# Kernel tuning notes

Measured on AMD Instinct MI355X. Metric: run time of the kernel, lower is better.

## Reference

```python
import jax, jax.numpy as jnp
import numpy as np
from jax import lax

B, T, F, H, L = 64, 2048, 128, 128, 2


def _lstm_layer(x, Wih, Whh, bih, bhh, h0, c0):
    """Single LSTM layer, torch gate order (i,f,g,o). x: [B,T,in] -> y: [B,T,H], hT, cT."""
    b = bih + bhh

    def step(carry, xt):
        h, c = carry
        gates = xt @ Wih.T + h @ Whh.T + b  # [B,4H]
        i, f, g, o = jnp.split(gates, 4, axis=-1)
        i = jax.nn.sigmoid(i)
        f = jax.nn.sigmoid(f)
        g = jnp.tanh(g)
        o = jax.nn.sigmoid(o)
        c = f * c + i * g
        h = o * jnp.tanh(c)
        return (h, c), h

    xs = jnp.swapaxes(x, 0, 1)  # [T,B,in]
    (hT, cT), ys = lax.scan(step, (h0, c0), xs)
    return jnp.swapaxes(ys, 0, 1), hT, cT


def setup_inputs() -> dict:
    key = jax.random.key(0)
    ks = jax.random.split(key, 20)
    s = 1.0 / np.sqrt(H)
    u = lambda k, shape: jax.random.uniform(k, shape, jnp.float32, -s, s)
    inp = {"x": jax.random.normal(ks[0], (B, T, F), jnp.float32)}
    i = 1
    for pre, in0 in (("enc", F), ("dec", H)):
        for l in range(L):
            d_in = in0 if l == 0 else H
            inp[f"{pre}_Wih{l}"] = u(ks[i], (4 * H, d_in)); i += 1
            inp[f"{pre}_Whh{l}"] = u(ks[i], (4 * H, H)); i += 1
            inp[f"{pre}_bih{l}"] = u(ks[i], (4 * H,)); i += 1
            inp[f"{pre}_bhh{l}"] = u(ks[i], (4 * H,)); i += 1
    inp["out_W"] = u(ks[i], (F, H)); i += 1
    inp["out_b"] = u(ks[i], (F,))
    return inp


def reference(x,
              enc_Wih0, enc_Whh0, enc_bih0, enc_bhh0,
              enc_Wih1, enc_Whh1, enc_bih1, enc_bhh1,
              dec_Wih0, dec_Whh0, dec_bih0, dec_bhh0,
              dec_Wih1, dec_Whh1, dec_bih1, dec_bhh1,
              out_W, out_b):
    z = jnp.zeros((x.shape[0], H), x.dtype)
    # encoder: 2 stacked layers, zero initial state
    y0, h0, c0 = _lstm_layer(x, enc_Wih0, enc_Whh0, enc_bih0, enc_bhh0, z, z)
    y1, h1, c1 = _lstm_layer(y0, enc_Wih1, enc_Whh1, enc_bih1, enc_bhh1, z, z)
    # decoder: zeros input, initial state = encoder final (h,c) per layer
    dec_in = jnp.zeros_like(x)  # valid since n_features == hidden_dim
    d0, _, _ = _lstm_layer(dec_in, dec_Wih0, dec_Whh0, dec_bih0, dec_bhh0, h0, c0)
    d1, _, _ = _lstm_layer(d0, dec_Wih1, dec_Whh1, dec_bih1, dec_bhh1, h1, c1)
    return d1 @ out_W.T + out_b
```

## Files before the change

kernel.cpp:

```cpp
#include <hip/hip_runtime.h>
#include <cstdint>
#include <cstddef>

typedef float    float4v __attribute__((ext_vector_type(4)));
typedef _Float16 f16x4   __attribute__((ext_vector_type(4)));
typedef _Float16 f16x8   __attribute__((ext_vector_type(8)));
typedef unsigned long long u64;
struct u64p { u64 a, b; };

#define DI __device__ __forceinline__

static const int Bsz = 64, Tlen = 2048, Hd = 128, G4 = 512;
static const int HSTR = 144;
static const int RING = 256;
static const int YSTR = 136;

DI float sigf_fast(float x) {
    float e = __builtin_amdgcn_exp2f(-1.442695041f * x);
    return __builtin_amdgcn_rcpf(1.f + e);
}
DI float tanhf_fast(float x) {
    float e = __builtin_amdgcn_exp2f(-2.885390082f * x);
    return 2.f * __builtin_amdgcn_rcpf(1.f + e) - 1.f;
}

DI void lds_barrier() {
    asm volatile("s_waitcnt lgkmcnt(0)\n\ts_barrier" ::: "memory");
}

DI void pin(f16x8& v) {
    float4v t = __builtin_bit_cast(float4v, v);
    asm volatile("" : "+v"(t));
    v = __builtin_bit_cast(f16x8, t);
}

DI f16x8 cvt8(const float* p) {
    float4v u = *(const float4v*)p;
    float4v w = *(const float4v*)(p + 4);
    f16x8 o;
    o[0] = (_Float16)u[0]; o[1] = (_Float16)u[1]; o[2] = (_Float16)u[2]; o[3] = (_Float16)u[3];
    o[4] = (_Float16)w[0]; o[5] = (_Float16)w[1]; o[6] = (_Float16)w[2]; o[7] = (_Float16)w[3];
    return o;
}

DI u64 ald64(const void* pp) {
    return __hip_atomic_load((const u64*)pp, __ATOMIC_RELAXED, __HIP_MEMORY_SCOPE_AGENT);
}
DI void ast16(void* pp, unsigned short v) {
    __hip_atomic_store((unsigned short*)pp, v, __ATOMIC_RELAXED, __HIP_MEMORY_SCOPE_AGENT);
}
DI unsigned int aldu32(const unsigned int* pp) {
    return __hip_atomic_load(pp, __ATOMIC_RELAXED, __HIP_MEMORY_SCOPE_AGENT);
}
DI void astu32(unsigned int* pp, unsigned int v) {
    __hip_atomic_store(pp, v, __ATOMIC_RELAXED, __HIP_MEMORY_SCOPE_AGENT);
}

template <bool P_HAS_XP, bool P_INIT, bool C_INIT, bool R3_OUT>
__global__ __launch_bounds__(512, 1) void lstm_fused4(
    const float* __restrict__ Up, const float* __restrict__ bip, const float* __restrict__ bhp,
    const float* __restrict__ php, const float* __restrict__ pcp,
    float* __restrict__ fhp, float* __restrict__ fcp,
    const float* __restrict__ Wc, const float* __restrict__ Uc,
    const float* __restrict__ bic, const float* __restrict__ bhc,
    const float* __restrict__ phc, const float* __restrict__ pcc,
    float* __restrict__ fhc, float* __restrict__ fcc,
    const float* __restrict__ Wx, const float* __restrict__ xin,
    const float* __restrict__ oW, const float* __restrict__ ob,
    float* __restrict__ outp,
    _Float16* __restrict__ PB,
    _Float16* __restrict__ X2,
    _Float16* __restrict__ X1,
    _Float16* __restrict__ Y1,
    unsigned int* __restrict__ prog,  unsigned int* __restrict__ prog2,
    unsigned int* __restrict__ prog3, unsigned int* __restrict__ prog4, int T)
{
    const int tid  = threadIdx.x;
    const int lane = tid & 63, w = tid >> 6;
    const int col  = lane & 15, quad = lane >> 4;
    const int b    = col & 3, s = col >> 2;
    const int role = blockIdx.x >> 4;
    const int p    = blockIdx.x & 15;
    const int bglob = p * 4 + b;
    const int j    = w * 16 + s * 4 + quad;
    const int NG   = T >> 3;

    __shared__ alignas(16) _Float16 Hl[2 * 4 * HSTR];
    __shared__ alignas(16) _Float16 Ylh[32 * YSTR];

    unsigned int* pr  = prog  + p * 16;
    unsigned int* pr2 = prog2 + p * 16;
    unsigned int* pr3 = P_HAS_XP ? prog3 + p * 16 : nullptr;
    unsigned int* pr4 = R3_OUT   ? prog4 + p * 16 : nullptr;

    if (role == 0) {
        f16x8 af[4][4];
#pragma unroll
        for (int mt = 0; mt < 4; mt++) {
            int urow = (col & 3) * 128 + (w * 16 + mt * 4 + (col >> 2));
            const float* ur = Up + (size_t)urow * 128;
#pragma unroll
            for (int kc = 0; kc < 4; kc++) af[mt][kc] = cvt8(ur + kc * 32 + quad * 8);
        }
#pragma unroll
        for (int mt = 0; mt < 4; mt++)
#pragma unroll
            for (int kc = 0; kc < 4; kc++) pin(af[mt][kc]);

        float bq[4];
#pragma unroll
        for (int q = 0; q < 4; q++) bq[q] = bip[q * 128 + j] + bhp[q * 128 + j];

        float c = 0.f, hv = 0.f;
        if (P_INIT) {
            c  = pcp[(size_t)bglob * 128 + j];
            hv = php[(size_t)bglob * 128 + j];
        }
        Hl[b * HSTR + j] = (_Float16)hv;
        __syncthreads();

        const _Float16* x1b = P_HAS_XP ? X1 + (size_t)bglob * RING * 512 + 4 * j : nullptr;
        unsigned short* pbp = (unsigned short*)PB + (size_t)bglob * RING * 128 + j;

        if constexpr (P_HAS_XP) {
            if (tid == 511) {
                unsigned int need = 16u; if (need > (unsigned int)T) need = (unsigned int)T;
                unsigned int psn = aldu32(pr3);
                while (psn < need) { __builtin_amdgcn_s_sleep(8); psn = aldu32(pr3); }
            }
            __syncthreads();
        }
        f16x4 xp = {};
        if (P_HAS_XP) xp = __builtin_bit_cast(f16x4, ald64(x1b));

        int cur = 0;
        for (int g = 0; g < NG; g++) {
#pragma unroll
            for (int k = 0; k < 8; k++) {
                const int t = g * 8 + k;
                f16x4 xpn = {};
                if (P_HAS_XP)
                    xpn = __builtin_bit_cast(f16x4, ald64(x1b + (size_t)((t + 1) & (RING - 1)) * 512));

                const _Float16* Hc = Hl + cur * (4 * HSTR);
                f16x8 bf[4];
#pragma unroll
                for (int kc = 0; kc < 4; kc++)
                    bf[kc] = *(const f16x8*)(Hc + b * HSTR + kc * 32 + quad * 8);

                float4v acc[4] = {};
#pragma unroll
                for (int kc = 0; kc < 4; kc++)
#pragma unroll
                    for (int mt = 0; mt < 4; mt++)
                        acc[mt] = __builtin_amdgcn_mfma_f32_16x16x32_f16(af[mt][kc], bf[kc], acc[mt], 0, 0, 0);

                float4v t0 = (s & 1) ? acc[1] : acc[0];
                float4v t1 = (s & 1) ? acc[3] : acc[2];
                float4v gg = (s & 2) ? t1 : t0;

                float g0 = gg[0] + bq[0], g1 = gg[1] + bq[1], g2 = gg[2] + bq[2], g3 = gg[3] + bq[3];
                if (P_HAS_XP) { g0 += (float)xp[0]; g1 += (float)xp[1]; g2 += (float)xp[2]; g3 += (float)xp[3]; }
                float iv = sigf_fast(g0), fv = sigf_fast(g1);
                float gv = tanhf_fast(g2), ov = sigf_fast(g3);
                c  = fv * c + iv * gv;
                hv = ov * tanhf_fast(c);

                _Float16 hf = (_Float16)hv;
                Hl[(cur ^ 1) * (4 * HSTR) + b * HSTR + j] = hf;
                ast16(pbp + (size_t)(t & (RING - 1)) * 128,
                      __builtin_bit_cast(unsigned short, hf));

                lds_barrier();
                xp = xpn;
                cur ^= 1;
            }
            if constexpr (P_HAS_XP) asm volatile("s_waitcnt vmcnt(2)" ::: "memory");
            else                    asm volatile("s_waitcnt vmcnt(1)" ::: "memory");
            if (tid == 0) astu32(pr, (unsigned int)(g * 8 + 7));
            if constexpr (P_HAS_XP) {
                if (tid == 511 && g + 1 < NG) {
                    unsigned int need = (unsigned int)(8 * (g + 1) + 16);
                    if (need > (unsigned int)T) need = (unsigned int)T;
                    unsigned int psn = aldu32(pr3);
                    while (psn < need) { __builtin_amdgcn_s_sleep(2); psn = aldu32(pr3); }
                }
                lds_barrier();
            }
        }

        asm volatile("s_waitcnt vmcnt(0)" ::: "memory");
        __syncthreads();
        if (tid == 0) astu32(pr, (unsigned int)T);

        fhp[(size_t)bglob * 128 + j] = hv;
        fcp[(size_t)bglob * 128 + j] = c;
    } else if (role == 1) {
        f16x8 afH[4][4];
#pragma unroll
        for (int mt = 0; mt < 4; mt++) {
            int urow = (col & 3) * 128 + (w * 16 + mt * 4 + (col >> 2));
            const float* ur = Uc + (size_t)urow * 128;
#pragma unroll
            for (int kc = 0; kc < 4; kc++) afH[mt][kc] = cvt8(ur + kc * 32 + quad * 8);
        }
#pragma unroll
        for (int mt = 0; mt < 4; mt++)
#pragma unroll
            for (int kc = 0; kc < 4; kc++) pin(afH[mt][kc]);

        float bq[4];
#pragma unroll
        for (int q = 0; q < 4; q++) bq[q] = bic[q * 128 + j] + bhc[q * 128 + j];

        float c = 0.f, hv = 0.f;
        if (C_INIT) {
            c  = pcc[(size_t)bglob * 128 + j];
            hv = phc[(size_t)bglob * 128 + j];
        }
        Hl[b * HSTR + j] = (_Float16)hv;

        if (tid == 511) {
            unsigned int need = 9u; if (need > (unsigned int)T) need = (unsigned int)T;
            unsigned int psn = aldu32(pr2);
            while (psn < need) { __builtin_amdgcn_s_sleep(8); psn = aldu32(pr2); }
        }
        __syncthreads();

        const _Float16* x2b = X2 + (size_t)bglob * RING * 512 + 4 * j;
        unsigned short* y1p = R3_OUT ? (unsigned short*)Y1 + (size_t)bglob * T * 128 + j : nullptr;
        f16x4 xp = __builtin_bit_cast(f16x4, ald64(x2b));

        int cur = 0;
        for (int g = 0; g < NG; g++) {
#pragma unroll
            for (int k = 0; k < 8; k++) {
                const int t = g * 8 + k;
                const int slot = (t + 1) & (RING - 1);
                f16x4 xpn = __builtin_bit_cast(f16x4, ald64(x2b + (size_t)slot * 512));

                const _Float16* Hc = Hl + cur * (4 * HSTR);
                f16x8 bf[4];
#pragma unroll
                for (int kc = 0; kc < 4; kc++)
                    bf[kc] = *(const f16x8*)(Hc + b * HSTR + kc * 32 + quad * 8);

                float4v acc[4] = {};
#pragma unroll
                for (int kc = 0; kc < 4; kc++)
#pragma unroll
                    for (int mt = 0; mt < 4; mt++)
                        acc[mt] = __builtin_amdgcn_mfma_f32_16x16x32_f16(afH[mt][kc], bf[kc], acc[mt], 0, 0, 0);

                float4v t0 = (s & 1) ? acc[1] : acc[0];
                float4v t1 = (s & 1) ? acc[3] : acc[2];
                float4v gg = (s & 2) ? t1 : t0;

                float g0 = gg[0] + bq[0] + (float)xp[0], g1 = gg[1] + bq[1] + (float)xp[1];
                float g2 = gg[2] + bq[2] + (float)xp[2], g3 = gg[3] + bq[3] + (float)xp[3];
                float iv = sigf_fast(g0), fv = sigf_fast(g1);
                float gv = tanhf_fast(g2), ov = sigf_fast(g3);
                c  = fv * c + iv * gv;
                hv = ov * tanhf_fast(c);

                _Float16 hf = (_Float16)hv;
                Hl[(cur ^ 1) * (4 * HSTR) + b * HSTR + j] = hf;
                if constexpr (R3_OUT)
                    ast16(y1p + (size_t)t * 128, __builtin_bit_cast(unsigned short, hf));

                lds_barrier();
                xp = xpn;
                cur ^= 1;
            }
            if constexpr (R3_OUT) {
                asm volatile("s_waitcnt vmcnt(2)" ::: "memory");
                if (tid == 0) astu32(pr4, (unsigned int)(g * 8 + 7));
            }
            if (tid == 511 && g + 1 < NG) {
                unsigned int need = (unsigned int)(8 * (g + 1) + 9);
                if (need > (unsigned int)T) need = (unsigned int)T;
                unsigned int psn = aldu32(pr2);
                while (psn < need) { __builtin_amdgcn_s_sleep(2); psn = aldu32(pr2); }
            }
            lds_barrier();
        }

        if constexpr (R3_OUT) {
            asm volatile("s_waitcnt vmcnt(0)" ::: "memory");
            __syncthreads();
            if (tid == 0) astu32(pr4, (unsigned int)T);
        }
        fhc[(size_t)bglob * 128 + j] = hv;
        fcc[(size_t)bglob * 128 + j] = c;
    } else if (role == 2) {
        f16x8 bw[4][4];
#pragma unroll
        for (int nt = 0; nt < 4; nt++) {
            int n = (w * 4 + nt) * 16 + col;
            int wrow = (n & 3) * 128 + (n >> 2);
            const float* Wr = Wc + (size_t)wrow * 128;
#pragma unroll
            for (int kc = 0; kc < 4; kc++) bw[nt][kc] = cvt8(Wr + kc * 32 + quad * 8);
        }
#pragma unroll
        for (int nt = 0; nt < 4; nt++)
#pragma unroll
            for (int kc = 0; kc < 4; kc++) pin(bw[nt][kc]);

        const int lrow = tid >> 4, lchunk = tid & 15;
        const int lb = lrow & 3, ltr = lrow >> 2;

        for (int g = 0; g < NG; g++) {
            if (tid == 0) {
                unsigned int need = (unsigned int)(g * 8 + 8);
                unsigned int psn = aldu32(pr);
                while (psn < need) { __builtin_amdgcn_s_sleep(4); psn = aldu32(pr); }
            }
            __syncthreads();
            {
                int slot = (g * 8 + ltr) & (RING - 1);
                const char* srcp = (const char*)(PB + ((size_t)(p * 4 + lb) * RING + slot) * 128 + lchunk * 8);
                u64 a0 = ald64(srcp);
                u64 a1 = ald64(srcp + 8);
                char* dst = (char*)&Ylh[lrow * YSTR + lchunk * 8];
                *(u64*)dst = a0;
                *(u64*)(dst + 8) = a1;
            }
            lds_barrier();

            float4v acc[2][4] = {};
#pragma unroll
            for (int kc = 0; kc < 4; kc++) {
                f16x8 a0 = *(const f16x8*)&Ylh[col * YSTR + kc * 32 + quad * 8];
                f16x8 a1 = *(const f16x8*)&Ylh[(16 + col) * YSTR + kc * 32 + quad * 8];
#pragma unroll
                for (int nt = 0; nt < 4; nt++) {
                    acc[0][nt] = __builtin_amdgcn_mfma_f32_16x16x32_f16(a0, bw[nt][kc], acc[0][nt], 0, 0, 0);
                    acc[1][nt] = __builtin_amdgcn_mfma_f32_16x16x32_f16(a1, bw[nt][kc], acc[1][nt], 0, 0, 0);
                }
            }
#pragma unroll
            for (int mt = 0; mt < 2; mt++)
#pragma unroll
                for (int nt = 0; nt < 4; nt++) {
                    int n = (w * 4 + nt) * 16 + col;
#pragma unroll
                    for (int r = 0; r < 4; r++) {
                        int m = mt * 16 + quad * 4 + r;
                        int bb = m & 3, trow = m >> 2;
                        int slot = (g * 8 + trow) & (RING - 1);
                        _Float16 hval = (_Float16)acc[mt][nt][r];
                        ast16(X2 + ((size_t)(p * 4 + bb) * RING + slot) * 512 + n,
                              __builtin_bit_cast(unsigned short, hval));
                    }
                }
            asm volatile("s_waitcnt vmcnt(0)" ::: "memory");
            __syncthreads();
            if (tid == 0) astu32(pr2, (unsigned int)(g * 8 + 8));
        }
    } else if constexpr (!R3_OUT) {
        f16x8 bw[4][4];
#pragma unroll
        for (int nt = 0; nt < 4; nt++) {
            int n = (w * 4 + nt) * 16 + col;
            int wrow = (n & 3) * 128 + (n >> 2);
            const float* Wr = Wx + (size_t)wrow * 128;
#pragma unroll
            for (int kc = 0; kc < 4; kc++) bw[nt][kc] = cvt8(Wr + kc * 32 + quad * 8);
        }
#pragma unroll
        for (int nt = 0; nt < 4; nt++)
#pragma unroll
            for (int kc = 0; kc < 4; kc++) pin(bw[nt][kc]);

        const int lrow = tid >> 4, lchunk = tid & 15;
        const int lb = lrow & 3, ltr = lrow >> 2;
        const float* xsrc = xin + (size_t)(p * 4 + lb) * T * 128 + lchunk * 8;

        for (int g = 0; g < NG; g++) {
            if (g >= 32 && tid == 0) {
                unsigned int need = (unsigned int)(8 * (g - 32));
                unsigned int psn = aldu32(pr);
                while (psn < need) { __builtin_amdgcn_s_sleep(4); psn = aldu32(pr); }
            }
            __syncthreads();
            {
                f16x8 xv = cvt8(xsrc + (size_t)(g * 8 + ltr) * 128);
                u64p w2 = __builtin_bit_cast(u64p, xv);
                char* dst = (char*)&Ylh[lrow * YSTR + lchunk * 8];
                *(u64*)dst = w2.a;
                *(u64*)(dst + 8) = w2.b;
            }
            lds_barrier();

            float4v acc[2][4] = {};
#pragma unroll
            for (int kc = 0; kc < 4; kc++) {
                f16x8 a0 = *(const f16x8*)&Ylh[col * YSTR + kc * 32 + quad * 8];
                f16x8 a1 = *(const f16x8*)&Ylh[(16 + col) * YSTR + kc * 32 + quad * 8];
#pragma unroll
                for (int nt = 0; nt < 4; nt++) {
                    acc[0][nt] = __builtin_amdgcn_mfma_f32_16x16x32_f16(a0, bw[nt][kc], acc[0][nt], 0, 0, 0);
                    acc[1][nt] = __builtin_amdgcn_mfma_f32_16x16x32_f16(a1, bw[nt][kc], acc[1][nt], 0, 0, 0);
                }
            }
#pragma unroll
            for (int mt = 0; mt < 2; mt++)
#pragma unroll
                for (int nt = 0; nt < 4; nt++) {
                    int n = (w * 4 + nt) * 16 + col;
#pragma unroll
                    for (int r = 0; r < 4; r++) {
                        int m = mt * 16 + quad * 4 + r;
                        int bb = m & 3, trow = m >> 2;
                        int slot = (g * 8 + trow) & (RING - 1);
                        _Float16 hval = (_Float16)acc[mt][nt][r];
                        ast16(X1 + ((size_t)(p * 4 + bb) * RING + slot) * 512 + n,
                              __builtin_bit_cast(unsigned short, hval));
                    }
                }
            asm volatile("s_waitcnt vmcnt(0)" ::: "memory");
            __syncthreads();
            if (tid == 0) astu32(pr3, (unsigned int)(g * 8 + 8));
        }
    } else {
        const int n = w * 16 + col;
        f16x8 bo[4];
#pragma unroll
        for (int kc = 0; kc < 4; kc++) bo[kc] = cvt8(oW + (size_t)n * 128 + kc * 32 + quad * 8);
#pragma unroll
        for (int kc = 0; kc < 4; kc++) pin(bo[kc]);
        const float bv = ob[n];

        const int lrow = tid >> 4, lchunk = tid & 15;
        const int lb = lrow & 3, ltr = lrow >> 2;

        for (int g = 0; g < NG; g++) {
            if (tid == 0) {
                unsigned int need = (unsigned int)(g * 8 + 8);
                unsigned int psn = aldu32(pr4);
                while (psn < need) { __builtin_amdgcn_s_sleep(4); psn = aldu32(pr4); }
            }
            __syncthreads();
            {
                const char* srcp = (const char*)(Y1 + ((size_t)(p * 4 + lb) * T + g * 8 + ltr) * 128 + lchunk * 8);
                u64 a0 = ald64(srcp);
                u64 a1 = ald64(srcp + 8);
                char* dst = (char*)&Ylh[lrow * YSTR + lchunk * 8];
                *(u64*)dst = a0;
                *(u64*)(dst + 8) = a1;
            }
            lds_barrier();

            float4v acc[2] = {};
#pragma unroll
            for (int kc = 0; kc < 4; kc++) {
                f16x8 a0 = *(const f16x8*)&Ylh[col * YSTR + kc * 32 + quad * 8];
                f16x8 a1 = *(const f16x8*)&Ylh[(16 + col) * YSTR + kc * 32 + quad * 8];
                acc[0] = __builtin_amdgcn_mfma_f32_16x16x32_f16(a0, bo[kc], acc[0], 0, 0, 0);
                acc[1] = __builtin_amdgcn_mfma_f32_16x16x32_f16(a1, bo[kc], acc[1], 0, 0, 0);
            }
#pragma unroll
            for (int mt = 0; mt < 2; mt++)
#pragma unroll
                for (int r = 0; r < 4; r++) {
                    int m = mt * 16 + quad * 4 + r;
                    int bb = m & 3, trow = m >> 2;
                    outp[((size_t)(p * 4 + bb) * T + g * 8 + trow) * 128 + n] = acc[mt][r] + bv;
                }
        }
    }
}

extern "C" void kernel_launch(void* const* d_in, const int* in_sizes, int n_in,
                              void* d_out, int out_size, void* d_ws, size_t ws_size,
                              hipStream_t stream)
{
    const float* x    = (const float*)d_in[0];
    const float* eW0  = (const float*)d_in[1];
    const float* eU0  = (const float*)d_in[2];
    const float* eb0i = (const float*)d_in[3];
    const float* eb0h = (const float*)d_in[4];
    const float* eW1  = (const float*)d_in[5];
    const float* eU1  = (const float*)d_in[6];
    const float* eb1i = (const float*)d_in[7];
    const float* eb1h = (const float*)d_in[8];
    const float* dU0  = (const float*)d_in[10];
    const float* db0i = (const float*)d_in[11];
    const float* db0h = (const float*)d_in[12];
    const float* dW1  = (const float*)d_in[13];
    const float* dU1  = (const float*)d_in[14];
    const float* db1i = (const float*)d_in[15];
    const float* db1h = (const float*)d_in[16];
    const float* oW   = (const float*)d_in[17];
    const float* ob   = (const float*)d_in[18];

    char* ws = (char*)d_ws;
    _Float16* X1  = (_Float16*)(ws);
    _Float16* X2A = (_Float16*)(ws + (16u << 20));
    _Float16* PBA = (_Float16*)(ws + (32u << 20));
    _Float16* X2B = (_Float16*)(ws + (36u << 20));
    _Float16* PBB = (_Float16*)(ws + (52u << 20));
    _Float16* Y1  = (_Float16*)(ws + (56u << 20));
    float*    fh0 = (float*)(ws + (88u << 20));
    float*    fc0 = fh0 + Bsz * Hd;
    float*    fh1 = fc0 + Bsz * Hd;
    float*    fc1 = fh1 + Bsz * Hd;
    unsigned int* pg = (unsigned int*)(ws + (88u << 20) + (1u << 17));
    unsigned int* progA  = pg + 0 * 256;
    unsigned int* prog2A = pg + 1 * 256;
    unsigned int* prog3A = pg + 2 * 256;
    unsigned int* progB  = pg + 3 * 256;
    unsigned int* prog2B = pg + 4 * 256;
    unsigned int* prog4B = pg + 5 * 256;

    hipMemsetAsync((void*)pg, 0, 8192, stream);

    lstm_fused4<true, false, false, false><<<dim3(64), dim3(512), 0, stream>>>(
        eU0, eb0i, eb0h, (const float*)nullptr, (const float*)nullptr, fh0, fc0,
        eW1, eU1, eb1i, eb1h, (const float*)nullptr, (const float*)nullptr, fh1, fc1,
        eW0, x,
        (const float*)nullptr, (const float*)nullptr, (float*)nullptr,
        PBA, X2A, X1, (_Float16*)nullptr,
        progA, prog2A, prog3A, (unsigned int*)nullptr, Tlen);

    lstm_fused4<false, true, true, true><<<dim3(64), dim3(512), 0, stream>>>(
        dU0, db0i, db0h, fh0, fc0, fh0, fc0,
        dW1, dU1, db1i, db1h, fh1, fc1, fh1, fc1,
        (const float*)nullptr, (const float*)nullptr,
        oW, ob, (float*)d_out,
        PBB, X2B, (_Float16*)nullptr, Y1,
        progB, prog2B, (unsigned int*)nullptr, prog4B, Tlen);
}
```

Baseline: 2.674 ms.

## Ring-buffer decoder output, vectorize projection stores, fold group sync into last step

```diff
diff --git a/kernel.cpp b/kernel.cpp
--- a/kernel.cpp
+++ b/kernel.cpp
@@ -43,9 +43,19 @@
     return o;
 }
 
+DI u64 pack4(float4v a) {
+    f16x4 h;
+    h[0] = (_Float16)a[0]; h[1] = (_Float16)a[1];
+    h[2] = (_Float16)a[2]; h[3] = (_Float16)a[3];
+    return __builtin_bit_cast(u64, h);
+}
+
 DI u64 ald64(const void* pp) {
     return __hip_atomic_load((const u64*)pp, __ATOMIC_RELAXED, __HIP_MEMORY_SCOPE_AGENT);
 }
+DI void ast64(void* pp, u64 v) {
+    __hip_atomic_store((u64*)pp, v, __ATOMIC_RELAXED, __HIP_MEMORY_SCOPE_AGENT);
+}
 DI void ast16(void* pp, unsigned short v) {
     __hip_atomic_store((unsigned short*)pp, v, __ATOMIC_RELAXED, __HIP_MEMORY_SCOPE_AGENT);
 }
@@ -57,7 +67,7 @@
 }
 
 template <bool P_HAS_XP, bool P_INIT, bool C_INIT, bool R3_OUT>
-__global__ __launch_bounds__(512, 1) void lstm_fused4(
+__global__ __launch_bounds__(512, 1) void lstm_fused5(
     const float* __restrict__ Up, const float* __restrict__ bip, const float* __restrict__ bhp,
     const float* __restrict__ php, const float* __restrict__ pcp,
     float* __restrict__ fhp, float* __restrict__ fcp,
@@ -73,7 +83,8 @@
     _Float16* __restrict__ X1,
     _Float16* __restrict__ Y1,
     unsigned int* __restrict__ prog,  unsigned int* __restrict__ prog2,
-    unsigned int* __restrict__ prog3, unsigned int* __restrict__ prog4, int T)
+    unsigned int* __restrict__ prog3, unsigned int* __restrict__ prog4,
+    unsigned int* __restrict__ prog5, int T)
 {
     const int tid  = threadIdx.x;
     const int lane = tid & 63, w = tid >> 6;
@@ -92,6 +103,7 @@
     unsigned int* pr2 = prog2 + p * 16;
     unsigned int* pr3 = P_HAS_XP ? prog3 + p * 16 : nullptr;
     unsigned int* pr4 = R3_OUT   ? prog4 + p * 16 : nullptr;
+    unsigned int* pr5 = R3_OUT   ? prog5 + p * 16 : nullptr;
 
     if (role == 0) {
         f16x8 af[4][4];
@@ -171,21 +183,22 @@
                 ast16(pbp + (size_t)(t & (RING - 1)) * 128,
                       __builtin_bit_cast(unsigned short, hf));
 
+                if (k == 7) {
+                    if constexpr (P_HAS_XP) asm volatile("s_waitcnt vmcnt(2)" ::: "memory");
+                    else                    asm volatile("s_waitcnt vmcnt(1)" ::: "memory");
+                    if (tid == 0) astu32(pr, (unsigned int)(g * 8 + 7));
+                    if constexpr (P_HAS_XP) {
+                        if (tid == 511 && g + 1 < NG) {
+                            unsigned int need = (unsigned int)(8 * (g + 1) + 16);
+                            if (need > (unsigned int)T) need = (unsigned int)T;
+                            unsigned int psn = aldu32(pr3);
+                            while (psn < need) { __builtin_amdgcn_s_sleep(2); psn = aldu32(pr3); }
+                        }
+                    }
+                }
                 lds_barrier();
                 xp = xpn;
                 cur ^= 1;
-            }
-            if constexpr (P_HAS_XP) asm volatile("s_waitcnt vmcnt(2)" ::: "memory");
-            else                    asm volatile("s_waitcnt vmcnt(1)" ::: "memory");
-            if (tid == 0) astu32(pr, (unsigned int)(g * 8 + 7));
-            if constexpr (P_HAS_XP) {
-                if (tid == 511 && g + 1 < NG) {
-                    unsigned int need = (unsigned int)(8 * (g + 1) + 16);
-                    if (need > (unsigned int)T) need = (unsigned int)T;
-                    unsigned int psn = aldu32(pr3);
-                    while (psn < need) { __builtin_amdgcn_s_sleep(2); psn = aldu32(pr3); }
-                }
-                lds_barrier();
             }
         }
 
@@ -228,7 +241,7 @@
         __syncthreads();
 
         const _Float16* x2b = X2 + (size_t)bglob * RING * 512 + 4 * j;
-        unsigned short* y1p = R3_OUT ? (unsigned short*)Y1 + (size_t)bglob * T * 128 + j : nullptr;
+        unsigned short* y1p = R3_OUT ? (unsigned short*)Y1 + (size_t)bglob * RING * 128 + j : nullptr;
         f16x4 xp = __builtin_bit_cast(f16x4, ald64(x2b));
 
         int cur = 0;
@@ -266,23 +279,32 @@
                 _Float16 hf = (_Float16)hv;
                 Hl[(cur ^ 1) * (4 * HSTR) + b * HSTR + j] = hf;
                 if constexpr (R3_OUT)
-                    ast16(y1p + (size_t)t * 128, __builtin_bit_cast(unsigned short, hf));
-
+                    ast16(y1p + (size_t)(t & (RING - 1)) * 128,
+                          __builtin_bit_cast(unsigned short, hf));
+
+                if (k == 7) {
+                    if constexpr (R3_OUT) {
+                        asm volatile("s_waitcnt vmcnt(2)" ::: "memory");
+                        if (tid == 0) astu32(pr4, (unsigned int)(g * 8 + 7));
+                    }
+                    if (tid == 511 && g + 1 < NG) {
+                        unsigned int need = (unsigned int)(8 * (g + 1) + 9);
+                        if (need > (unsigned int)T) need = (unsigned int)T;
+                        unsigned int psn = aldu32(pr2);
+                        while (psn < need) { __builtin_amdgcn_s_sleep(2); psn = aldu32(pr2); }
+                        if constexpr (R3_OUT) {
+                            if (g + 1 >= 32) {
+                                unsigned int need5 = (unsigned int)(8 * (g + 1 - 32) + 8);
+                                unsigned int p5 = aldu32(pr5);
+                                while (p5 < need5) { __builtin_amdgcn_s_sleep(2); p5 = aldu32(pr5); }
+                            }
+                        }
+                    }
+                }
                 lds_barrier();
                 xp = xpn;
                 cur ^= 1;
             }
-            if constexpr (R3_OUT) {
-                asm volatile("s_waitcnt vmcnt(2)" ::: "memory");
-                if (tid == 0) astu32(pr4, (unsigned int)(g * 8 + 7));
-            }
-            if (tid == 511 && g + 1 < NG) {
-                unsigned int need = (unsigned int)(8 * (g + 1) + 9);
-                if (need > (unsigned int)T) need = (unsigned int)T;
-                unsigned int psn = aldu32(pr2);
-                while (psn < need) { __builtin_amdgcn_s_sleep(2); psn = aldu32(pr2); }
-            }
-            lds_barrier();
         }
 
         if constexpr (R3_OUT) {
@@ -331,29 +353,26 @@
             float4v acc[2][4] = {};
 #pragma unroll
             for (int kc = 0; kc < 4; kc++) {
-                f16x8 a0 = *(const f16x8*)&Ylh[col * YSTR + kc * 32 + quad * 8];
-                f16x8 a1 = *(const f16x8*)&Ylh[(16 + col) * YSTR + kc * 32 + quad * 8];
+                f16x8 y0 = *(const f16x8*)&Ylh[col * YSTR + kc * 32 + quad * 8];
+                f16x8 y1t = *(const f16x8*)&Ylh[(16 + col) * YSTR + kc * 32 + quad * 8];
 #pragma unroll
                 for (int nt = 0; nt < 4; nt++) {
-                    acc[0][nt] = __builtin_amdgcn_mfma_f32_16x16x32_f16(a0, bw[nt][kc], acc[0][nt], 0, 0, 0);
-                    acc[1][nt] = __builtin_amdgcn_mfma_f32_16x16x32_f16(a1, bw[nt][kc], acc[1][nt], 0, 0, 0);
-                }
-            }
-#pragma unroll
-            for (int mt = 0; mt < 2; mt++)
-#pragma unroll
-                for (int nt = 0; nt < 4; nt++) {
-                    int n = (w * 4 + nt) * 16 + col;
-#pragma unroll
-                    for (int r = 0; r < 4; r++) {
-                        int m = mt * 16 + quad * 4 + r;
-                        int bb = m & 3, trow = m >> 2;
-                        int slot = (g * 8 + trow) & (RING - 1);
-                        _Float16 hval = (_Float16)acc[mt][nt][r];
-                        ast16(X2 + ((size_t)(p * 4 + bb) * RING + slot) * 512 + n,
-                              __builtin_bit_cast(unsigned short, hval));
-                    }
-                }
+                    acc[0][nt] = __builtin_amdgcn_mfma_f32_16x16x32_f16(bw[nt][kc], y0,  acc[0][nt], 0, 0, 0);
+                    acc[1][nt] = __builtin_amdgcn_mfma_f32_16x16x32_f16(bw[nt][kc], y1t, acc[1][nt], 0, 0, 0);
+                }
+            }
+            {
+                const int bb = col & 3;
+#pragma unroll
+                for (int mt = 0; mt < 2; mt++) {
+                    int trow = mt * 4 + (col >> 2);
+                    int slot = (g * 8 + trow) & (RING - 1);
+                    _Float16* dst = X2 + ((size_t)(p * 4 + bb) * RING + slot) * 512 + (w * 4) * 16 + quad * 4;
+#pragma unroll
+                    for (int nt = 0; nt < 4; nt++)
+                        ast64(dst + nt * 16, pack4(acc[mt][nt]));
+                }
+            }
             asm volatile("s_waitcnt vmcnt(0)" ::: "memory");
             __syncthreads();
             if (tid == 0) astu32(pr2, (unsigned int)(g * 8 + 8));
@@ -396,41 +415,37 @@
             float4v acc[2][4] = {};
 #pragma unroll
             for (int kc = 0; kc < 4; kc++) {
-                f16x8 a0 = *(const f16x8*)&Ylh[col * YSTR + kc * 32 + quad * 8];
-                f16x8 a1 = *(const f16x8*)&Ylh[(16 + col) * YSTR + kc * 32 + quad * 8];
+                f16x8 y0 = *(const f16x8*)&Ylh[col * YSTR + kc * 32 + quad * 8];
+                f16x8 y1t = *(const f16x8*)&Ylh[(16 + col) * YSTR + kc * 32 + quad * 8];
 #pragma unroll
                 for (int nt = 0; nt < 4; nt++) {
-                    acc[0][nt] = __builtin_amdgcn_mfma_f32_16x16x32_f16(a0, bw[nt][kc], acc[0][nt], 0, 0, 0);
-                    acc[1][nt] = __builtin_amdgcn_mfma_f32_16x16x32_f16(a1, bw[nt][kc], acc[1][nt], 0, 0, 0);
-                }
-            }
-#pragma unroll
-            for (int mt = 0; mt < 2; mt++)
-#pragma unroll
-                for (int nt = 0; nt < 4; nt++) {
-                    int n = (w * 4 + nt) * 16 + col;
-#pragma unroll
-                    for (int r = 0; r < 4; r++) {
-                        int m = mt * 16 + quad * 4 + r;
-                        int bb = m & 3, trow = m >> 2;
-                        int slot = (g * 8 + trow) & (RING - 1);
-                        _Float16 hval = (_Float16)acc[mt][nt][r];
-                        ast16(X1 + ((size_t)(p * 4 + bb) * RING + slot) * 512 + n,
-                              __builtin_bit_cast(unsigned short, hval));
-                    }
-                }
+                    acc[0][nt] = __builtin_amdgcn_mfma_f32_16x16x32_f16(bw[nt][kc], y0,  acc[0][nt], 0, 0, 0);
+                    acc[1][nt] = __builtin_amdgcn_mfma_f32_16x16x32_f16(bw[nt][kc], y1t, acc[1][nt], 0, 0, 0);
+                }
+            }
+            {
+                const int bb = col & 3;
+#pragma unroll
+                for (int mt = 0; mt < 2; mt++) {
+                    int trow = mt * 4 + (col >> 2);
+                    int slot = (g * 8 + trow) & (RING - 1);
+                    _Float16* dst = X1 + ((size_t)(p * 4 + bb) * RING + slot) * 512 + (w * 4) * 16 + quad * 4;
+#pragma unroll
+                    for (int nt = 0; nt < 4; nt++)
+                        ast64(dst + nt * 16, pack4(acc[mt][nt]));
+                }
+            }
             asm volatile("s_waitcnt vmcnt(0)" ::: "memory");
             __syncthreads();
             if (tid == 0) astu32(pr3, (unsigned int)(g * 8 + 8));
         }
     } else {
-        const int n = w * 16 + col;
         f16x8 bo[4];
 #pragma unroll
-        for (int kc = 0; kc < 4; kc++) bo[kc] = cvt8(oW + (size_t)n * 128 + kc * 32 + quad * 8);
+        for (int kc = 0; kc < 4; kc++) bo[kc] = cvt8(oW + (size_t)(w * 16 + col) * 128 + kc * 32 + quad * 8);
 #pragma unroll
         for (int kc = 0; kc < 4; kc++) pin(bo[kc]);
-        const float bv = ob[n];
+        float4v bv4 = *(const float4v*)(ob + w * 16 + quad * 4);
 
         const int lrow = tid >> 4, lchunk = tid & 15;
         const int lb = lrow & 3, ltr = lrow >> 2;
@@ -443,7 +458,8 @@
             }
             __syncthreads();
             {
-                const char* srcp = (const char*)(Y1 + ((size_t)(p * 4 + lb) * T + g * 8 + ltr) * 128 + lchunk * 8);
+                int slot = (g * 8 + ltr) & (RING - 1);
+                const char* srcp = (const char*)(Y1 + ((size_t)(p * 4 + lb) * RING + slot) * 128 + lchunk * 8);
                 u64 a0 = ald64(srcp);
                 u64 a1 = ald64(srcp + 8);
                 char* dst = (char*)&Ylh[lrow * YSTR + lchunk * 8];
@@ -451,23 +467,26 @@
                 *(u64*)(dst + 8) = a1;
             }
             lds_barrier();
+            if (tid == 0) astu32(pr5, (unsigned int)(g * 8 + 8));
 
             float4v acc[2] = {};
 #pragma unroll
             for (int kc = 0; kc < 4; kc++) {
-                f16x8 a0 = *(const f16x8*)&Ylh[col * YSTR + kc * 32 + quad * 8];
-                f16x8 a1 = *(const f16x8*)&Ylh[(16 + col) * YSTR + kc * 32 + quad * 8];
-                acc[0] = __builtin_amdgcn_mfma_f32_16x16x32_f16(a0, bo[kc], acc[0], 0, 0, 0);
-                acc[1] = __builtin_amdgcn_mfma_f32_16x16x32_f16(a1, bo[kc], acc[1], 0, 0, 0);
-            }
-#pragma unroll
-            for (int mt = 0; mt < 2; mt++)
-#pragma unroll
-                for (int r = 0; r < 4; r++) {
-                    int m = mt * 16 + quad * 4 + r;
-                    int bb = m & 3, trow = m >> 2;
-                    outp[((size_t)(p * 4 + bb) * T + g * 8 + trow) * 128 + n] = acc[mt][r] + bv;
-                }
+                f16x8 y0 = *(const f16x8*)&Ylh[col * YSTR + kc * 32 + quad * 8];
+                f16x8 y1t = *(const f16x8*)&Ylh[(16 + col) * YSTR + kc * 32 + quad * 8];
+                acc[0] = __builtin_amdgcn_mfma_f32_16x16x32_f16(bo[kc], y0,  acc[0], 0, 0, 0);
+                acc[1] = __builtin_amdgcn_mfma_f32_16x16x32_f16(bo[kc], y1t, acc[1], 0, 0, 0);
+            }
+            {
+                const int bb = col & 3;
+#pragma unroll
+                for (int mt = 0; mt < 2; mt++) {
+                    int trow = mt * 4 + (col >> 2);
+                    float4v v = acc[mt];
+                    v[0] += bv4[0]; v[1] += bv4[1]; v[2] += bv4[2]; v[3] += bv4[3];
+                    *(float4v*)(outp + ((size_t)(p * 4 + bb) * T + g * 8 + trow) * 128 + w * 16 + quad * 4) = v;
+                }
+            }
         }
     }
 }
@@ -501,7 +520,7 @@
     _Float16* PBA = (_Float16*)(ws + (32u << 20));
     _Float16* X2B = (_Float16*)(ws + (36u << 20));
     _Float16* PBB = (_Float16*)(ws + (52u << 20));
-    _Float16* Y1  = (_Float16*)(ws + (56u << 20));
+    _Float16* Y1R = (_Float16*)(ws + (56u << 20));
     float*    fh0 = (float*)(ws + (88u << 20));
     float*    fc0 = fh0 + Bsz * Hd;
     float*    fh1 = fc0 + Bsz * Hd;
@@ -513,22 +532,23 @@
     unsigned int* progB  = pg + 3 * 256;
     unsigned int* prog2B = pg + 4 * 256;
     unsigned int* prog4B = pg + 5 * 256;
+    unsigned int* prog5B = pg + 6 * 256;
 
     hipMemsetAsync((void*)pg, 0, 8192, stream);
 
-    lstm_fused4<true, false, false, false><<<dim3(64), dim3(512), 0, stream>>>(
+    lstm_fused5<true, false, false, false><<<dim3(64), dim3(512), 0, stream>>>(
         eU0, eb0i, eb0h, (const float*)nullptr, (const float*)nullptr, fh0, fc0,
         eW1, eU1, eb1i, eb1h, (const float*)nullptr, (const float*)nullptr, fh1, fc1,
         eW0, x,
         (const float*)nullptr, (const float*)nullptr, (float*)nullptr,
         PBA, X2A, X1, (_Float16*)nullptr,
-        progA, prog2A, prog3A, (unsigned int*)nullptr, Tlen);
-
-    lstm_fused4<false, true, true, true><<<dim3(64), dim3(512), 0, stream>>>(
+        progA, prog2A, prog3A, (unsigned int*)nullptr, (unsigned int*)nullptr, Tlen);
+
+    lstm_fused5<false, true, true, true><<<dim3(64), dim3(512), 0, stream>>>(
         dU0, db0i, db0h, fh0, fc0, fh0, fc0,
         dW1, dU1, db1i, db1h, fh1, fc1, fh1, fc1,
         (const float*)nullptr, (const float*)nullptr,
         oW, ob, (float*)d_out,
-        PBB, X2B, (_Float16*)nullptr, Y1,
-        progB, prog2B, (unsigned int*)nullptr, prog4B, Tlen);
-}
+        PBB, X2B, (_Float16*)nullptr, Y1R,
+        progB, prog2B, (unsigned int*)nullptr, prog4B, prog5B, Tlen);
+}
```

After: 2.576 ms. -3.6%, faster.
